# Kernel optimization log

Hardware: AMD Instinct MI355X
Metric: run time of the kernel (lower is better)

The kernel has to match this reference:

```python
import jax, jax.numpy as jnp
import numpy as np

N = 100000      # nodes
E = 1000000     # edges
H_DIM = 124     # node embedding dim
CLS_DIM = 4     # node class-logit dim (H_DIM + CLS_DIM = in_features = 128)
POLAR_DIM = 2   # edge_pred_features
HIDDEN = 256
OUT = 2
LN_EPS = 1e-5


def setup_inputs() -> dict:
    key = jax.random.key(0)
    ks = jax.random.split(key, 10)
    in_dim = 2 * (H_DIM + CLS_DIM) + POLAR_DIM  # 258
    return {
        "h": jax.random.normal(ks[0], (N, H_DIM), dtype=jnp.float32),
        "cls": jax.random.normal(ks[1], (N, CLS_DIM), dtype=jnp.float32),
        "polar": jax.random.normal(ks[2], (E, POLAR_DIM), dtype=jnp.float32),
        "src": jax.random.randint(ks[3], (E,), 0, N, dtype=jnp.int64),
        "dst": jax.random.randint(ks[4], (E,), 0, N, dtype=jnp.int64),
        # parameters (PyTorch Linear default-ish init scale)
        "W1": jax.random.normal(ks[5], (in_dim, HIDDEN), dtype=jnp.float32) * (1.0 / np.sqrt(in_dim)),
        "b1": jnp.zeros((HIDDEN,), dtype=jnp.float32),
        "gamma": jnp.ones((HIDDEN,), dtype=jnp.float32),
        "beta": jnp.zeros((HIDDEN,), dtype=jnp.float32),
        "W2": jax.random.normal(ks[6], (HIDDEN, OUT), dtype=jnp.float32) * (1.0 / np.sqrt(HIDDEN)),
        "b2": jnp.zeros((OUT,), dtype=jnp.float32),
    }


def reference(h, cls, polar, src, dst, W1, b1, gamma, beta, W2, b2):
    # softmax over class logits per node (same math as softmax on gathered
    # edge copies, but computed once per node)
    cls_sm = jax.nn.softmax(cls, axis=1)                  # [N, CLS_DIM]
    # gather src/dst node features along edges
    x = jnp.concatenate(
        [h[src], cls_sm[src], polar, h[dst], cls_sm[dst]], axis=1
    )                                                     # [E, 258]
    z = x @ W1 + b1                                        # [E, HIDDEN]
    # LayerNorm
    mu = jnp.mean(z, axis=-1, keepdims=True)
    var = jnp.mean(jnp.square(z - mu), axis=-1, keepdims=True)
    z = (z - mu) * jax.lax.rsqrt(var + LN_EPS) * gamma + beta
    z = jax.nn.relu(z)
    # dropout is identity in eval mode
    score = z @ W2 + b2                                    # [E, OUT]
    return score
```

## Files before the change

### kernel.cpp

```cpp
#include <hip/hip_runtime.h>
#include <hip/hip_bf16.h>

#define NN 100000
#define EE 1000000
#define H_DIM 124
#define PCOLS 512
#define LDK 136

typedef float f32x4 __attribute__((ext_vector_type(4)));
typedef short bf16x8 __attribute__((ext_vector_type(8)));
typedef _Float16 h2 __attribute__((ext_vector_type(2)));

__device__ __forceinline__ unsigned short f2bf(float f) {
    unsigned int x = __float_as_uint(f);
    unsigned int r = (x + 0x7FFFu + ((x >> 16) & 1u)) >> 16;
    return (unsigned short)r;
}

__device__ __forceinline__ float fdot2(h2 a, h2 b, float c) {
#if __has_builtin(__builtin_amdgcn_fdot2)
    return __builtin_amdgcn_fdot2(a, b, c, false);
#else
    return c + (float)a[0] * (float)b[0] + (float)a[1] * (float)b[1];
#endif
}

struct alignas(16) H8 { h2 p[4]; };

__global__ __launch_bounds__(256) void build_tables(const float* __restrict__ h,
                                                    const float* __restrict__ cls,
                                                    const float* __restrict__ W1,
                                                    unsigned short* __restrict__ F,
                                                    unsigned short* __restrict__ W1T) {
    int tid = blockIdx.x * 256 + threadIdx.x;
    if (tid < NN * 128) {
        int n = tid >> 7, j = tid & 127;
        float v;
        if (j < H_DIM) {
            v = h[n * H_DIM + j];
        } else {
            const float* c = cls + n * 4;
            float c0 = c[0], c1 = c[1], c2 = c[2], c3 = c[3];
            float m = fmaxf(fmaxf(c0, c1), fmaxf(c2, c3));
            float e0 = __expf(c0 - m), e1 = __expf(c1 - m), e2 = __expf(c2 - m), e3 = __expf(c3 - m);
            float s = e0 + e1 + e2 + e3;
            int jj = j - H_DIM;
            float ev = (jj == 0) ? e0 : (jj == 1) ? e1 : (jj == 2) ? e2 : e3;
            v = ev / s;
        }
        F[tid] = f2bf(v);
    } else if (tid < NN * 128 + PCOLS * 128) {
        int t2 = tid - NN * 128;
        int j = t2 >> 7, k = t2 & 127;
        int row = (j < 256) ? k : (130 + k);
        int col = (j < 256) ? j : (j - 256);
        W1T[t2] = f2bf(W1[row * 256 + col]);
    }
}

__global__ __launch_bounds__(256) void p_gemm(const unsigned short* __restrict__ F,
                                              const unsigned short* __restrict__ W1T,
                                              _Float16* __restrict__ P) {
    __shared__ unsigned short As[64 * LDK];
    __shared__ unsigned short Bs[128 * LDK];
    const int m0 = blockIdx.x * 64;
    const int t = threadIdx.x;

    #pragma unroll
    for (int it = 0; it < 4; ++it) {
        int chunk = t + it * 256;
        int r = chunk >> 4, c = chunk & 15;
        float4 v = make_float4(0.f, 0.f, 0.f, 0.f);
        int row = m0 + r;
        if (row < NN) v = *(const float4*)(F + row * 128 + c * 8);
        *(float4*)(&As[r * LDK + c * 8]) = v;
    }

    const int wave = t >> 6, lane = t & 63;
    const int wm = wave & 1, wn = wave >> 1;
    const int lm = lane & 15, quad = lane >> 4;

    for (int cchunk = 0; cchunk < 4; ++cchunk) {
        const int n0 = cchunk * 128;
        if (cchunk) __syncthreads();
        #pragma unroll
        for (int it = 0; it < 8; ++it) {
            int chunk = t + it * 256;
            int r = chunk >> 4, c = chunk & 15;
            float4 v = *(const float4*)(W1T + (n0 + r) * 128 + c * 8);
            *(float4*)(&Bs[r * LDK + c * 8]) = v;
        }
        __syncthreads();

        f32x4 acc[2][4];
        #pragma unroll
        for (int mt = 0; mt < 2; ++mt)
            #pragma unroll
            for (int nt = 0; nt < 4; ++nt)
                acc[mt][nt] = (f32x4){0.f, 0.f, 0.f, 0.f};

        #pragma unroll
        for (int s = 0; s < 4; ++s) {
            int k0 = s * 32 + quad * 8;
            bf16x8 a[2], b[4];
            #pragma unroll
            for (int mt = 0; mt < 2; ++mt)
                a[mt] = *(const bf16x8*)(&As[(wm * 32 + mt * 16 + lm) * LDK + k0]);
            #pragma unroll
            for (int nt = 0; nt < 4; ++nt)
                b[nt] = *(const bf16x8*)(&Bs[(wn * 64 + nt * 16 + lm) * LDK + k0]);
            #pragma unroll
            for (int mt = 0; mt < 2; ++mt)
                #pragma unroll
                for (int nt = 0; nt < 4; ++nt)
                    acc[mt][nt] = __builtin_amdgcn_mfma_f32_16x16x32_bf16(a[mt], b[nt], acc[mt][nt], 0, 0, 0);
        }

        #pragma unroll
        for (int mt = 0; mt < 2; ++mt) {
            #pragma unroll
            for (int nt = 0; nt < 4; ++nt) {
                int col = n0 + wn * 64 + nt * 16 + lm;
                #pragma unroll
                for (int r = 0; r < 4; ++r) {
                    int row = m0 + wm * 32 + mt * 16 + quad * 4 + r;
                    if (row < NN) P[(size_t)row * PCOLS + col] = (_Float16)acc[mt][nt][r];
                }
            }
        }
    }
}

#define K3_BLOCKS 2048
#define K3_WAVES (K3_BLOCKS * 4)

__global__ __launch_bounds__(256) void edge_kernel(const _Float16* __restrict__ P,
                                                   const int* __restrict__ src,
                                                   const int* __restrict__ dst,
                                                   const float* __restrict__ polar,
                                                   const float* __restrict__ W1,
                                                   const float* __restrict__ b1,
                                                   const float* __restrict__ gamma,
                                                   const float* __restrict__ beta,
                                                   const float* __restrict__ W2,
                                                   const float* __restrict__ b2,
                                                   float* __restrict__ out) {
    const int lane = threadIdx.x & 63;
    const int il   = lane & 31;
    const int half = lane >> 5;
    const int wid  = blockIdx.x * 4 + (threadIdx.x >> 6);
    const int jb   = il * 8;

    h2 w0c[4], w1c[4], b1c[4], gc[4], bc[4], w2ac[4], w2bc[4];
    #pragma unroll
    for (int p = 0; p < 4; ++p) {
        int j = jb + 2 * p;
        float2 a0 = *(const float2*)(W1 + 128 * 256 + j);
        float2 a1 = *(const float2*)(W1 + 129 * 256 + j);
        float2 ab = *(const float2*)(b1 + j);
        float2 ag = *(const float2*)(gamma + j);
        float2 ae = *(const float2*)(beta + j);
        float4 w2v = *(const float4*)(W2 + 2 * j);
        w0c[p]  = (h2){(_Float16)a0.x, (_Float16)a0.y};
        w1c[p]  = (h2){(_Float16)a1.x, (_Float16)a1.y};
        b1c[p]  = (h2){(_Float16)ab.x, (_Float16)ab.y};
        gc[p]   = (h2){(_Float16)ag.x, (_Float16)ag.y};
        bc[p]   = (h2){(_Float16)ae.x, (_Float16)ae.y};
        w2ac[p] = (h2){(_Float16)w2v.x, (_Float16)w2v.z};
        w2bc[p] = (h2){(_Float16)w2v.y, (_Float16)w2v.w};
    }
    const float b20 = b2[0], b21 = b2[1];
    const h2 onep = (h2){(_Float16)1.0f, (_Float16)1.0f};
    const h2 zerop = (h2){(_Float16)0.0f, (_Float16)0.0f};

    const int stride = K3_WAVES * 2;
    const int base = wid * 2;

    int s0, d0, s1, d1;
    float q00, q01, q10, q11;
    {
        int b = base, e = (b < EE) ? (b + half) : 0;
        s0 = src[e]; d0 = dst[e];
        float2 pw = *(const float2*)(polar + 2 * e);
        q00 = pw.x; q01 = pw.y;
    }
    {
        int b = base + stride, e = (b < EE) ? (b + half) : 0;
        s1 = src[e]; d1 = dst[e];
        float2 pw = *(const float2*)(polar + 2 * e);
        q10 = pw.x; q11 = pw.y;
    }
    H8 ps = *(const H8*)(P + (size_t)s0 * PCOLS + jb);
    H8 pd = *(const H8*)(P + (size_t)d0 * PCOLS + 256 + jb);

    for (int e = base; e < EE; e += stride) {
        int s2, d2; float q20, q21;
        {
            int b = e + 2 * stride, ec = (b < EE) ? (b + half) : 0;
            s2 = src[ec]; d2 = dst[ec];
            float2 pw = *(const float2*)(polar + 2 * ec);
            q20 = pw.x; q21 = pw.y;
        }
        H8 psn = *(const H8*)(P + (size_t)s1 * PCOLS + jb);
        H8 pdn = *(const H8*)(P + (size_t)d1 * PCOLS + 256 + jb);

        h2 p0h = (h2){(_Float16)q00, (_Float16)q00};
        h2 p1h = (h2){(_Float16)q01, (_Float16)q01};
        h2 z[4];
        float sum = 0.f, ss = 0.f;
        #pragma unroll
        for (int p = 0; p < 4; ++p) {
            h2 c = w0c[p] * p0h + (w1c[p] * p1h + b1c[p]);
            z[p] = (ps.p[p] + pd.p[p]) + c;
            sum = fdot2(z[p], onep, sum);
            ss  = fdot2(z[p], z[p], ss);
        }
        #pragma unroll
        for (int off = 16; off; off >>= 1) {
            sum += __shfl_xor(sum, off);
            ss  += __shfl_xor(ss, off);
        }
        float mu   = sum * (1.0f / 256.0f);
        float var  = ss * (1.0f / 256.0f) - mu * mu;
        float rstd = rsqrtf(var + 1e-5f);
        h2 muh = (h2){(_Float16)mu, (_Float16)mu};
        h2 rsh = (h2){(_Float16)rstd, (_Float16)rstd};

        float o0 = 0.f, o1 = 0.f;
        #pragma unroll
        for (int p = 0; p < 4; ++p) {
            h2 t = (z[p] - muh) * rsh;
            h2 u = t * gc[p] + bc[p];
            u = __builtin_elementwise_max(u, zerop);
            o0 = fdot2(u, w2ac[p], o0);
            o1 = fdot2(u, w2bc[p], o1);
        }
        #pragma unroll
        for (int off = 16; off; off >>= 1) {
            o0 += __shfl_xor(o0, off);
            o1 += __shfl_xor(o1, off);
        }
        if (il == 0) {
            *(float2*)(out + 2 * (e + half)) = make_float2(o0 + b20, o1 + b21);
        }

        s0 = s1; d0 = d1; q00 = q10; q01 = q11;
        s1 = s2; d1 = d2; q10 = q20; q11 = q21;
        ps = psn; pd = pdn;
    }
}

extern "C" void kernel_launch(void* const* d_in, const int* in_sizes, int n_in,
                              void* d_out, int out_size, void* d_ws, size_t ws_size,
                              hipStream_t stream) {
    const float* h     = (const float*)d_in[0];
    const float* cls   = (const float*)d_in[1];
    const float* polar = (const float*)d_in[2];
    const int*   src   = (const int*)d_in[3];
    const int*   dst   = (const int*)d_in[4];
    const float* W1    = (const float*)d_in[5];
    const float* b1    = (const float*)d_in[6];
    const float* gamma = (const float*)d_in[7];
    const float* beta  = (const float*)d_in[8];
    const float* W2    = (const float*)d_in[9];
    const float* b2    = (const float*)d_in[10];
    float* out = (float*)d_out;

    char* ws = (char*)d_ws;
    _Float16*       P   = (_Float16*)ws;
    unsigned short* F   = (unsigned short*)(ws + 102400000);
    unsigned short* W1T = (unsigned short*)(ws + 128000000);

    build_tables<<<50256, 256, 0, stream>>>(h, cls, W1, F, W1T);

    p_gemm<<<1563, 256, 0, stream>>>(F, W1T, P);

    edge_kernel<<<K3_BLOCKS, 256, 0, stream>>>(P, src, dst, polar, W1, b1, gamma, beta, W2, b2, out);
}
```

Measured before the change: 325.3 us.

## Fuse node feature conversion into P GEMM and stage outputs through LDS

```diff
diff --git a/kernel.cpp b/kernel.cpp
--- a/kernel.cpp
+++ b/kernel.cpp
@@ -6,6 +6,7 @@
 #define H_DIM 124
 #define PCOLS 512
 #define LDK 136
+#define CW 132
 
 typedef float f32x4 __attribute__((ext_vector_type(4)));
 typedef short bf16x8 __attribute__((ext_vector_type(8)));
@@ -15,6 +16,13 @@
     unsigned int x = __float_as_uint(f);
     unsigned int r = (x + 0x7FFFu + ((x >> 16) & 1u)) >> 16;
     return (unsigned short)r;
+}
+__device__ __forceinline__ unsigned int pk2bf(float a, float b) {
+    return (unsigned int)f2bf(a) | ((unsigned int)f2bf(b) << 16);
+}
+__device__ __forceinline__ unsigned int pk2h(float a, float b) {
+    h2 v = (h2){(_Float16)a, (_Float16)b};
+    return __builtin_bit_cast(unsigned int, v);
 }
 
 __device__ __forceinline__ float fdot2(h2 a, h2 b, float c) {
@@ -27,58 +35,65 @@
 
 struct alignas(16) H8 { h2 p[4]; };
 
-__global__ __launch_bounds__(256) void build_tables(const float* __restrict__ h,
-                                                    const float* __restrict__ cls,
-                                                    const float* __restrict__ W1,
-                                                    unsigned short* __restrict__ F,
-                                                    unsigned short* __restrict__ W1T) {
-    int tid = blockIdx.x * 256 + threadIdx.x;
-    if (tid < NN * 128) {
-        int n = tid >> 7, j = tid & 127;
-        float v;
-        if (j < H_DIM) {
-            v = h[n * H_DIM + j];
-        } else {
-            const float* c = cls + n * 4;
-            float c0 = c[0], c1 = c[1], c2 = c[2], c3 = c[3];
-            float m = fmaxf(fmaxf(c0, c1), fmaxf(c2, c3));
-            float e0 = __expf(c0 - m), e1 = __expf(c1 - m), e2 = __expf(c2 - m), e3 = __expf(c3 - m);
-            float s = e0 + e1 + e2 + e3;
-            int jj = j - H_DIM;
-            float ev = (jj == 0) ? e0 : (jj == 1) ? e1 : (jj == 2) ? e2 : e3;
-            v = ev / s;
-        }
-        F[tid] = f2bf(v);
-    } else if (tid < NN * 128 + PCOLS * 128) {
-        int t2 = tid - NN * 128;
-        int j = t2 >> 7, k = t2 & 127;
-        int row = (j < 256) ? k : (130 + k);
-        int col = (j < 256) ? j : (j - 256);
-        W1T[t2] = f2bf(W1[row * 256 + col]);
-    }
-}
-
-__global__ __launch_bounds__(256) void p_gemm(const unsigned short* __restrict__ F,
+__global__ __launch_bounds__(256) void build_w1t(const float* __restrict__ W1,
+                                                 unsigned short* __restrict__ W1T) {
+    int t2 = blockIdx.x * 256 + threadIdx.x;
+    int j = t2 >> 7, k = t2 & 127;
+    int row = (j < 256) ? k : (130 + k);
+    int col = (j < 256) ? j : (j - 256);
+    W1T[t2] = f2bf(W1[row * 256 + col]);
+}
+
+__global__ __launch_bounds__(256) void p_gemm(const float* __restrict__ h,
+                                              const float* __restrict__ cls,
                                               const unsigned short* __restrict__ W1T,
                                               _Float16* __restrict__ P) {
-    __shared__ unsigned short As[64 * LDK];
-    __shared__ unsigned short Bs[128 * LDK];
+    __shared__ alignas(16) unsigned short As[64 * LDK];
+    __shared__ alignas(16) unsigned short Bs[128 * LDK];
+    float* Cs = (float*)&Bs[0];
     const int m0 = blockIdx.x * 64;
     const int t = threadIdx.x;
 
     #pragma unroll
     for (int it = 0; it < 4; ++it) {
         int chunk = t + it * 256;
-        int r = chunk >> 4, c = chunk & 15;
-        float4 v = make_float4(0.f, 0.f, 0.f, 0.f);
+        int r = chunk >> 4, c8 = chunk & 15;
         int row = m0 + r;
-        if (row < NN) v = *(const float4*)(F + row * 128 + c * 8);
-        *(float4*)(&As[r * LDK + c * 8]) = v;
-    }
+        unsigned int w0 = 0, w1 = 0, w2 = 0, w3 = 0;
+        if (row < NN) {
+            if (c8 < 15) {
+                const float* hp = h + (size_t)row * H_DIM + c8 * 8;
+                float4 v0 = *(const float4*)(hp);
+                float4 v1 = *(const float4*)(hp + 4);
+                w0 = pk2bf(v0.x, v0.y); w1 = pk2bf(v0.z, v0.w);
+                w2 = pk2bf(v1.x, v1.y); w3 = pk2bf(v1.z, v1.w);
+            } else {
+                float4 v0 = *(const float4*)(h + (size_t)row * H_DIM + 120);
+                float4 c = *(const float4*)(cls + (size_t)row * 4);
+                float m = fmaxf(fmaxf(c.x, c.y), fmaxf(c.z, c.w));
+                float e0 = __expf(c.x - m), e1 = __expf(c.y - m);
+                float e2 = __expf(c.z - m), e3 = __expf(c.w - m);
+                float inv = 1.0f / (e0 + e1 + e2 + e3);
+                w0 = pk2bf(v0.x, v0.y); w1 = pk2bf(v0.z, v0.w);
+                w2 = pk2bf(e0 * inv, e1 * inv); w3 = pk2bf(e2 * inv, e3 * inv);
+            }
+        }
+        *(uint4*)(&As[r * LDK + c8 * 8]) = make_uint4(w0, w1, w2, w3);
+    }
+    __syncthreads();
 
     const int wave = t >> 6, lane = t & 63;
     const int wm = wave & 1, wn = wave >> 1;
     const int lm = lane & 15, quad = lane >> 4;
+
+    bf16x8 afrag[4][2];
+    #pragma unroll
+    for (int s = 0; s < 4; ++s) {
+        int k0 = s * 32 + quad * 8;
+        #pragma unroll
+        for (int mt = 0; mt < 2; ++mt)
+            afrag[s][mt] = *(const bf16x8*)(&As[(wm * 32 + mt * 16 + lm) * LDK + k0]);
+    }
 
     for (int cchunk = 0; cchunk < 4; ++cchunk) {
         const int n0 = cchunk * 128;
@@ -102,10 +117,7 @@
         #pragma unroll
         for (int s = 0; s < 4; ++s) {
             int k0 = s * 32 + quad * 8;
-            bf16x8 a[2], b[4];
-            #pragma unroll
-            for (int mt = 0; mt < 2; ++mt)
-                a[mt] = *(const bf16x8*)(&As[(wm * 32 + mt * 16 + lm) * LDK + k0]);
+            bf16x8 b[4];
             #pragma unroll
             for (int nt = 0; nt < 4; ++nt)
                 b[nt] = *(const bf16x8*)(&Bs[(wn * 64 + nt * 16 + lm) * LDK + k0]);
@@ -113,20 +125,33 @@
             for (int mt = 0; mt < 2; ++mt)
                 #pragma unroll
                 for (int nt = 0; nt < 4; ++nt)
-                    acc[mt][nt] = __builtin_amdgcn_mfma_f32_16x16x32_bf16(a[mt], b[nt], acc[mt][nt], 0, 0, 0);
-        }
-
-        #pragma unroll
-        for (int mt = 0; mt < 2; ++mt) {
+                    acc[mt][nt] = __builtin_amdgcn_mfma_f32_16x16x32_bf16(afrag[s][mt], b[nt], acc[mt][nt], 0, 0, 0);
+        }
+        __syncthreads();
+
+        #pragma unroll
+        for (int mt = 0; mt < 2; ++mt)
             #pragma unroll
             for (int nt = 0; nt < 4; ++nt) {
-                int col = n0 + wn * 64 + nt * 16 + lm;
+                int col = wn * 64 + nt * 16 + lm;
+                int rb  = wm * 32 + mt * 16 + quad * 4;
                 #pragma unroll
-                for (int r = 0; r < 4; ++r) {
-                    int row = m0 + wm * 32 + mt * 16 + quad * 4 + r;
-                    if (row < NN) P[(size_t)row * PCOLS + col] = (_Float16)acc[mt][nt][r];
-                }
+                for (int r = 0; r < 4; ++r)
+                    Cs[(rb + r) * CW + col] = acc[mt][nt][r];
             }
+        __syncthreads();
+
+        #pragma unroll
+        for (int it = 0; it < 4; ++it) {
+            int chunk = t + it * 256;
+            int r = chunk >> 4, c8 = chunk & 15;
+            float4 a = *(const float4*)(Cs + r * CW + c8 * 8);
+            float4 b = *(const float4*)(Cs + r * CW + c8 * 8 + 4);
+            uint4 o = make_uint4(pk2h(a.x, a.y), pk2h(a.z, a.w),
+                                 pk2h(b.x, b.y), pk2h(b.z, b.w));
+            int row = m0 + r;
+            if (row < NN)
+                *(uint4*)(P + (size_t)row * PCOLS + n0 + c8 * 8) = o;
         }
     }
 }
@@ -268,12 +293,11 @@
 
     char* ws = (char*)d_ws;
     _Float16*       P   = (_Float16*)ws;
-    unsigned short* F   = (unsigned short*)(ws + 102400000);
-    unsigned short* W1T = (unsigned short*)(ws + 128000000);
-
-    build_tables<<<50256, 256, 0, stream>>>(h, cls, W1, F, W1T);
-
-    p_gemm<<<1563, 256, 0, stream>>>(F, W1T, P);
+    unsigned short* W1T = (unsigned short*)(ws + 102400000);
+
+    build_w1t<<<256, 256, 0, stream>>>(W1, W1T);
+
+    p_gemm<<<1563, 256, 0, stream>>>(h, cls, W1T, P);
 
     edge_kernel<<<K3_BLOCKS, 256, 0, stream>>>(P, src, dst, polar, W1, b1, gamma, beta, W2, b2, out);
 }
```

New measurement: 303.1 us. -6.8%, faster.
